# Kernel tuning notes

Measured on AMD Instinct MI355X. Metric: run time of the kernel, lower is better.

The kernel has to match this reference:

```python
import jax, jax.numpy as jnp
import numpy as np

N_NODES = 10000
N_EDGES = 320000


def _graph_conv(x, W, b, src, dst, n):
    # DGL GraphConv, norm='both': D_out^{-1/2} on src side, aggregate, D_in^{-1/2} on dst side,
    # then linear + bias. Degrees clamped at 1 (allow_zero_in_degree=True).
    ones = jnp.ones(src.shape[0], dtype=x.dtype)
    deg_out = jnp.clip(jax.ops.segment_sum(ones, src, num_segments=n), 1.0)
    deg_in = jnp.clip(jax.ops.segment_sum(ones, dst, num_segments=n), 1.0)
    h = x * jax.lax.rsqrt(deg_out)[:, None]          # [n, f] scaled source feats
    agg = jax.ops.segment_sum(h[src], dst, num_segments=n)  # gather + scatter-add
    agg = agg * jax.lax.rsqrt(deg_in)[:, None]
    return agg @ W + b


def setup_inputs() -> dict:
    key = jax.random.key(0)
    ks = jax.random.split(key, 8)
    in_dim, h1, h2 = 512, 256, 128
    features = jax.random.normal(ks[0], (N_NODES, in_dim), dtype=jnp.float32)
    src = jax.random.randint(ks[1], (N_EDGES,), 0, N_NODES)
    dst = jax.random.randint(ks[2], (N_EDGES,), 0, N_NODES)
    noise = jax.random.normal(ks[3], (N_NODES, h2), dtype=jnp.float32)
    W1 = jax.random.normal(ks[4], (in_dim, h1), dtype=jnp.float32) / np.sqrt(in_dim)
    b1 = jnp.zeros((h1,), dtype=jnp.float32)
    W2 = jax.random.normal(ks[5], (h1, h2), dtype=jnp.float32) / np.sqrt(h1)
    b2 = jnp.zeros((h2,), dtype=jnp.float32)
    W3 = jax.random.normal(ks[6], (h1, h2), dtype=jnp.float32) / np.sqrt(h1)
    b3 = jnp.zeros((h2,), dtype=jnp.float32)
    return {"features": features, "src": src, "dst": dst, "noise": noise,
            "W1": W1, "b1": b1, "W2": W2, "b2": b2, "W3": W3, "b3": b3}


def reference(features, src, dst, noise, W1, b1, W2, b2, W3, b3):
    n = features.shape[0]
    h = jax.nn.relu(_graph_conv(features, W1, b1, src, dst, n))
    mean = _graph_conv(h, W2, b2, src, dst, n)
    log_std = _graph_conv(h, W3, b3, src, dst, n)
    z = mean + noise * jnp.exp(log_std)              # reparameterization
    adj_rec = jax.nn.sigmoid(z @ z.T)                # inner-product decoder [N, N]
    return adj_rec
```

## Files before the change

kernel.cpp:

```cpp
#include <hip/hip_runtime.h>
#include <hip/hip_fp16.h>


#define NN 10000
#define NE 320000
#define FD 512
#define H1 256
#define H2 128

typedef _Float16 half8 __attribute__((ext_vector_type(8)));
typedef float f32x4 __attribute__((ext_vector_type(4)));

__device__ __forceinline__ void acc4(float4& a, const float4 v) {
    a.x += v.x; a.y += v.y; a.z += v.z; a.w += v.w;
}

__global__ void k_zero(int* __restrict__ p, int n) {
    int i = blockIdx.x * blockDim.x + threadIdx.x;
    if (i < n) p[i] = 0;
}

__global__ void k_count(const int* __restrict__ src, const int* __restrict__ dst,
                        int* __restrict__ co, int* __restrict__ ci) {
    int e = blockIdx.x * blockDim.x + threadIdx.x;
    if (e < NE) {
        atomicAdd(&co[src[e]], 1);
        atomicAdd(&ci[dst[e]], 1);
    }
}

__global__ __launch_bounds__(1024) void k_scan(const int* __restrict__ ci, const int* __restrict__ co,
                                               int* __restrict__ row_ptr, int* __restrict__ cursor,
                                               float* __restrict__ rs_in, float* __restrict__ rs_out) {
    __shared__ int sm[1024];
    int tid = threadIdx.x;
    const int CH = (NN + 1023) / 1024;
    int base = tid * CH;
    int local[CH];
    int s = 0;
    #pragma unroll
    for (int i = 0; i < CH; ++i) {
        int idx = base + i;
        local[i] = s;
        if (idx < NN) s += ci[idx];
    }
    sm[tid] = s;
    __syncthreads();
    for (int off = 1; off < 1024; off <<= 1) {
        int v = (tid >= off) ? sm[tid - off] : 0;
        __syncthreads();
        sm[tid] += v;
        __syncthreads();
    }
    int excl = sm[tid] - s;
    #pragma unroll
    for (int i = 0; i < CH; ++i) {
        int idx = base + i;
        if (idx < NN) row_ptr[idx] = excl + local[i];
    }
    if (tid == 1023) row_ptr[NN] = sm[1023];
    for (int i = tid; i < NN; i += 1024) {
        int a = ci[i], b = co[i];
        rs_in[i]  = rsqrtf((float)(a > 1 ? a : 1));
        rs_out[i] = rsqrtf((float)(b > 1 ? b : 1));
        cursor[i] = 0;
    }
}

__global__ void k_bucket(const int* __restrict__ src, const int* __restrict__ dst,
                         const int* __restrict__ row_ptr, int* __restrict__ cursor,
                         int* __restrict__ esrc) {
    int e = blockIdx.x * blockDim.x + threadIdx.x;
    if (e < NE) {
        int d = dst[e];
        int p = row_ptr[d] + atomicAdd(&cursor[d], 1);
        esrc[p] = src[e];
    }
}

__global__ __launch_bounds__(256) void k_gemm(
    const float* __restrict__ A, int lda, int M, int K,
    const float* __restrict__ B0, const float* __restrict__ B1, int ldb, int nsplit,
    const float* __restrict__ bias0, const float* __restrict__ bias1,
    const float* __restrict__ ascale, float* __restrict__ C, int ldc) {
    __shared__ __align__(16) float As[16][64];
    __shared__ __align__(16) float Bs[16][64];
    int tid = threadIdx.x;
    int bm = blockIdx.x * 64;
    int bn = blockIdx.y * 64;
    const float* Bp; const float* bp; int bcol;
    if (bn < nsplit) { Bp = B0; bp = bias0; bcol = bn; }
    else             { Bp = B1; bp = bias1; bcol = bn - nsplit; }
    int tm = tid >> 4, tn = tid & 15;
    float acc[4][4] = {};
    int arow = tid >> 2;
    int akq  = tid & 3;
    int brow = tid >> 4;
    int bq   = tid & 15;
    int garow = bm + arow;
    const float* Aptr = (garow < M) ? (A + (size_t)garow * lda) : nullptr;
    float ascl = (ascale && garow < M) ? ascale[garow] : 1.0f;
    for (int k0 = 0; k0 < K; k0 += 16) {
        float4 av = {0.f, 0.f, 0.f, 0.f};
        if (Aptr) av = *(const float4*)(Aptr + k0 + akq * 4);
        av.x *= ascl; av.y *= ascl; av.z *= ascl; av.w *= ascl;
        float4 bv = *(const float4*)(Bp + (size_t)(k0 + brow) * ldb + bcol + bq * 4);
        __syncthreads();
        As[akq * 4 + 0][arow] = av.x;
        As[akq * 4 + 1][arow] = av.y;
        As[akq * 4 + 2][arow] = av.z;
        As[akq * 4 + 3][arow] = av.w;
        *(float4*)&Bs[brow][bq * 4] = bv;
        __syncthreads();
        #pragma unroll
        for (int kk = 0; kk < 16; ++kk) {
            float4 a = *(const float4*)&As[kk][tm * 4];
            float4 b = *(const float4*)&Bs[kk][tn * 4];
            float ar[4] = {a.x, a.y, a.z, a.w};
            float br[4] = {b.x, b.y, b.z, b.w};
            #pragma unroll
            for (int i = 0; i < 4; ++i)
                #pragma unroll
                for (int j = 0; j < 4; ++j)
                    acc[i][j] += ar[i] * br[j];
        }
    }
    float bvv[4];
    #pragma unroll
    for (int j = 0; j < 4; ++j) bvv[j] = bp ? bp[bcol + tn * 4 + j] : 0.0f;
    #pragma unroll
    for (int i = 0; i < 4; ++i) {
        int row = bm + tm * 4 + i;
        if (row < M) {
            float4 v;
            v.x = acc[i][0] + bvv[0];
            v.y = acc[i][1] + bvv[1];
            v.z = acc[i][2] + bvv[2];
            v.w = acc[i][3] + bvv[3];
            *(float4*)(C + (size_t)row * ldc + bn + tn * 4) = v;
        }
    }
}

template <bool FIRST>
__global__ __launch_bounds__(256) void k_agg(const float* __restrict__ in, float* __restrict__ out,
                                             const int* __restrict__ esrc, const int* __restrict__ row_ptr,
                                             const float* __restrict__ rs_in, const float* __restrict__ rs_out,
                                             const float* __restrict__ bias) {
    int node = (blockIdx.x * blockDim.x + threadIdx.x) >> 6;
    int lane = threadIdx.x & 63;
    if (node >= NN) return;
    int beg = row_ptr[node], end = row_ptr[node + 1];
    float4 acc = {0.f, 0.f, 0.f, 0.f};
    int e = beg;
    for (; e + 4 <= end; e += 4) {
        int s0 = esrc[e + 0], s1 = esrc[e + 1], s2 = esrc[e + 2], s3 = esrc[e + 3];
        float4 v0 = ((const float4*)(in + (size_t)s0 * H1))[lane];
        float4 v1 = ((const float4*)(in + (size_t)s1 * H1))[lane];
        float4 v2 = ((const float4*)(in + (size_t)s2 * H1))[lane];
        float4 v3 = ((const float4*)(in + (size_t)s3 * H1))[lane];
        acc4(acc, v0); acc4(acc, v1); acc4(acc, v2); acc4(acc, v3);
    }
    for (; e < end; ++e) {
        float4 v0 = ((const float4*)(in + (size_t)esrc[e] * H1))[lane];
        acc4(acc, v0);
    }
    float si = rs_in[node];
    float4 r;
    r.x = acc.x * si; r.y = acc.y * si; r.z = acc.z * si; r.w = acc.w * si;
    if (FIRST) {
        float4 bb = ((const float4*)bias)[lane];
        float so = rs_out[node];
        r.x = fmaxf(r.x + bb.x, 0.f) * so;
        r.y = fmaxf(r.y + bb.y, 0.f) * so;
        r.z = fmaxf(r.z + bb.z, 0.f) * so;
        r.w = fmaxf(r.w + bb.w, 0.f) * so;
    }
    ((float4*)(out + (size_t)node * H1))[lane] = r;
}

__global__ void k_z(const float* __restrict__ ml, const float* __restrict__ noise,
                    _Float16* __restrict__ z) {
    int i = blockIdx.x * blockDim.x + threadIdx.x;
    if (i < NN * H2) {
        int r = i >> 7, c = i & 127;
        float mean = ml[(size_t)r * 256 + c];
        float ls   = ml[(size_t)r * 256 + 128 + c];
        z[i] = (_Float16)(mean + noise[i] * __expf(ls));
    }
}

__global__ __launch_bounds__(256) void k_decoder(const _Float16* __restrict__ Z, float* __restrict__ out) {
    __shared__ __align__(16) _Float16 As[128][72];
    __shared__ __align__(16) _Float16 Bs[128][72];
    int tid = threadIdx.x;
    int lane = tid & 63;
    int w = tid >> 6;
    int wrow = (w >> 1) * 64;
    int wcol = (w & 1) * 64;
    int rowBase = blockIdx.y * 128;
    int colBase = blockIdx.x * 128;
    f32x4 acc[4][4] = {};
    for (int s = 0; s < 2; ++s) {
        __syncthreads();
        #pragma unroll
        for (int i = 0; i < 4; ++i) {
            int lin = i * 256 + tid;
            int r = lin >> 3, c = lin & 7;
            int4 v = {0, 0, 0, 0};
            int gr = rowBase + r;
            if (gr < NN) v = *(const int4*)(Z + (size_t)gr * H2 + s * 64 + c * 8);
            *(int4*)&As[r][c * 8] = v;
            int4 u = {0, 0, 0, 0};
            int gc = colBase + r;
            if (gc < NN) u = *(const int4*)(Z + (size_t)gc * H2 + s * 64 + c * 8);
            *(int4*)&Bs[r][c * 8] = u;
        }
        __syncthreads();
        #pragma unroll
        for (int kk = 0; kk < 2; ++kk) {
            int kof = kk * 32 + ((lane >> 4) << 3);
            half8 a[4], b[4];
            #pragma unroll
            for (int f = 0; f < 4; ++f) a[f] = *(const half8*)&As[wrow + f * 16 + (lane & 15)][kof];
            #pragma unroll
            for (int f = 0; f < 4; ++f) b[f] = *(const half8*)&Bs[wcol + f * 16 + (lane & 15)][kof];
            #pragma unroll
            for (int i = 0; i < 4; ++i)
                #pragma unroll
                for (int j = 0; j < 4; ++j)
                    acc[i][j] = __builtin_amdgcn_mfma_f32_16x16x32_f16(a[i], b[j], acc[i][j], 0, 0, 0);
        }
    }
    #pragma unroll
    for (int i = 0; i < 4; ++i) {
        int row0 = rowBase + wrow + i * 16 + ((lane >> 4) << 2);
        #pragma unroll
        for (int j = 0; j < 4; ++j) {
            int col = colBase + wcol + j * 16 + (lane & 15);
            if (col < NN) {
                #pragma unroll
                for (int r = 0; r < 4; ++r) {
                    int row = row0 + r;
                    if (row < NN) {
                        float x = acc[i][j][r];
                        float sg = 1.0f / (1.0f + __expf(-x));
                        __builtin_nontemporal_store(sg, out + (size_t)row * NN + col);
                    }
                }
            }
        }
    }
}

extern "C" void kernel_launch(void* const* d_in, const int* in_sizes, int n_in,
                              void* d_out, int out_size, void* d_ws, size_t ws_size,
                              hipStream_t stream) {
    const float* features = (const float*)d_in[0];
    const int*   src      = (const int*)d_in[1];
    const int*   dst      = (const int*)d_in[2];
    const float* noise    = (const float*)d_in[3];
    const float* W1 = (const float*)d_in[4];
    const float* b1 = (const float*)d_in[5];
    const float* W2 = (const float*)d_in[6];
    const float* b2 = (const float*)d_in[7];
    const float* W3 = (const float*)d_in[8];
    const float* b3 = (const float*)d_in[9];
    float* out = (float*)d_out;
    (void)in_sizes; (void)n_in; (void)out_size; (void)ws_size;

    char* ws = (char*)d_ws;
    size_t off = 0;
    auto alloc = [&](size_t bytes) -> void* {
        void* p = ws + off;
        off += (bytes + 255) & ~(size_t)255;
        return p;
    };
    int* degc_out = (int*)alloc(NN * sizeof(int));
    int* degc_in  = (int*)alloc(NN * sizeof(int));
    int* row_ptr  = (int*)alloc((NN + 1) * sizeof(int));
    int* cursor   = (int*)alloc(NN * sizeof(int));
    int* esrc     = (int*)alloc(NE * sizeof(int));
    float* rs_out = (float*)alloc(NN * sizeof(float));
    float* rs_in  = (float*)alloc(NN * sizeof(float));
    float* bufA   = (float*)alloc((size_t)NN * H1 * sizeof(float));
    float* bufB   = (float*)alloc((size_t)NN * H1 * sizeof(float));
    _Float16* Zh  = (_Float16*)alloc((size_t)NN * H2 * sizeof(_Float16));

    k_zero<<<(NN + 255) / 256, 256, 0, stream>>>(degc_out, NN);
    k_zero<<<(NN + 255) / 256, 256, 0, stream>>>(degc_in, NN);
    k_count<<<(NE + 255) / 256, 256, 0, stream>>>(src, dst, degc_out, degc_in);
    k_scan<<<1, 1024, 0, stream>>>(degc_in, degc_out, row_ptr, cursor, rs_in, rs_out);
    k_bucket<<<(NE + 255) / 256, 256, 0, stream>>>(src, dst, row_ptr, cursor, esrc);

    k_gemm<<<dim3((NN + 63) / 64, H1 / 64), 256, 0, stream>>>(
        features, FD, NN, FD, W1, nullptr, H1, H1, nullptr, nullptr, rs_out, bufA, H1);
    k_agg<true><<<NN / 4, 256, 0, stream>>>(bufA, bufB, esrc, row_ptr, rs_in, rs_out, b1);
    k_agg<false><<<NN / 4, 256, 0, stream>>>(bufB, bufA, esrc, row_ptr, rs_in, nullptr, nullptr);
    k_gemm<<<dim3((NN + 63) / 64, 4), 256, 0, stream>>>(
        bufA, H1, NN, H1, W2, W3, H2, H2, b2, b3, nullptr, bufB, 256);
    k_z<<<(NN * H2 + 255) / 256, 256, 0, stream>>>(bufB, noise, Zh);
    k_decoder<<<dim3((NN + 127) / 128, (NN + 127) / 128), 256, 0, stream>>>(Zh, out);
}
```

Baseline: 686.0 us.

## Replace FP32 SIMT GEMMs with split-FP16 MFMA GEMMs using pre-transposed weights

Replaces the scalar FP32 tiled GEMM with an MFMA-based kernel. Each FP32 operand is split into high and low FP16 halves and three 16x16x32 f16 MFMAs per tile pair recover near-FP32 accuracy. A new kernel pre-transposes and splits W1 and the concatenated W2/W3 into FP16 hi/lo arrays and merges the biases. The two degree-zeroing launches are also fused into one. This trades triple MFMA work and an extra cast launch for much higher matrix throughput than FP32 FMA loops.

New measurement: 660.7 us. -3.7%, faster.

```diff
diff --git a/kernel.cpp b/kernel.cpp
--- a/kernel.cpp
+++ b/kernel.cpp
@@ -9,15 +9,16 @@
 #define H2 128
 
 typedef _Float16 half8 __attribute__((ext_vector_type(8)));
+typedef _Float16 half4 __attribute__((ext_vector_type(4)));
 typedef float f32x4 __attribute__((ext_vector_type(4)));
 
 __device__ __forceinline__ void acc4(float4& a, const float4 v) {
     a.x += v.x; a.y += v.y; a.z += v.z; a.w += v.w;
 }
 
-__global__ void k_zero(int* __restrict__ p, int n) {
+__global__ void k_zero2(int* __restrict__ a, int* __restrict__ b, int n) {
     int i = blockIdx.x * blockDim.x + threadIdx.x;
-    if (i < n) p[i] = 0;
+    if (i < n) { a[i] = 0; b[i] = 0; }
 }
 
 __global__ void k_count(const int* __restrict__ src, const int* __restrict__ dst,
@@ -78,66 +79,107 @@
     }
 }
 
-__global__ __launch_bounds__(256) void k_gemm(
-    const float* __restrict__ A, int lda, int M, int K,
-    const float* __restrict__ B0, const float* __restrict__ B1, int ldb, int nsplit,
-    const float* __restrict__ bias0, const float* __restrict__ bias1,
-    const float* __restrict__ ascale, float* __restrict__ C, int ldc) {
-    __shared__ __align__(16) float As[16][64];
-    __shared__ __align__(16) float Bs[16][64];
+__global__ void k_castW(const float* __restrict__ W1, const float* __restrict__ W2,
+                        const float* __restrict__ W3, const float* __restrict__ b2,
+                        const float* __restrict__ b3,
+                        _Float16* __restrict__ W1Th, _Float16* __restrict__ W1Tl,
+                        _Float16* __restrict__ WcTh, _Float16* __restrict__ WcTl,
+                        float* __restrict__ biasC) {
+    int idx = blockIdx.x * blockDim.x + threadIdx.x;
+    if (idx < FD * H1) {
+        int k = idx >> 8, n = idx & 255;
+        float v = W1[idx];
+        _Float16 h = (_Float16)v;
+        W1Th[n * FD + k] = h;
+        W1Tl[n * FD + k] = (_Float16)(v - (float)h);
+    } else if (idx < FD * H1 + H1 * H1) {
+        int j = idx - FD * H1;
+        int k = j >> 8, n = j & 255;
+        float v = (n < H2) ? W2[k * H2 + n] : W3[k * H2 + (n - H2)];
+        _Float16 h = (_Float16)v;
+        WcTh[n * H1 + k] = h;
+        WcTl[n * H1 + k] = (_Float16)(v - (float)h);
+        if (k == 0) biasC[n] = (n < H2) ? b2[n] : b3[n - H2];
+    }
+}
+
+template <int K>
+__global__ __launch_bounds__(256) void k_gemm16(
+    const float* __restrict__ A, const float* __restrict__ ascale,
+    const _Float16* __restrict__ BTh, const _Float16* __restrict__ BTl,
+    const float* __restrict__ bias, float* __restrict__ C, int M) {
+    __shared__ __align__(16) _Float16 Ahs[64][72];
+    __shared__ __align__(16) _Float16 Als[64][72];
+    __shared__ __align__(16) _Float16 Bhs[64][72];
+    __shared__ __align__(16) _Float16 Bls[64][72];
     int tid = threadIdx.x;
-    int bm = blockIdx.x * 64;
-    int bn = blockIdx.y * 64;
-    const float* Bp; const float* bp; int bcol;
-    if (bn < nsplit) { Bp = B0; bp = bias0; bcol = bn; }
-    else             { Bp = B1; bp = bias1; bcol = bn - nsplit; }
-    int tm = tid >> 4, tn = tid & 15;
-    float acc[4][4] = {};
-    int arow = tid >> 2;
-    int akq  = tid & 3;
-    int brow = tid >> 4;
-    int bq   = tid & 15;
-    int garow = bm + arow;
-    const float* Aptr = (garow < M) ? (A + (size_t)garow * lda) : nullptr;
-    float ascl = (ascale && garow < M) ? ascale[garow] : 1.0f;
-    for (int k0 = 0; k0 < K; k0 += 16) {
-        float4 av = {0.f, 0.f, 0.f, 0.f};
-        if (Aptr) av = *(const float4*)(Aptr + k0 + akq * 4);
-        av.x *= ascl; av.y *= ascl; av.z *= ascl; av.w *= ascl;
-        float4 bv = *(const float4*)(Bp + (size_t)(k0 + brow) * ldb + bcol + bq * 4);
-        __syncthreads();
-        As[akq * 4 + 0][arow] = av.x;
-        As[akq * 4 + 1][arow] = av.y;
-        As[akq * 4 + 2][arow] = av.z;
-        As[akq * 4 + 3][arow] = av.w;
-        *(float4*)&Bs[brow][bq * 4] = bv;
-        __syncthreads();
-        #pragma unroll
-        for (int kk = 0; kk < 16; ++kk) {
-            float4 a = *(const float4*)&As[kk][tm * 4];
-            float4 b = *(const float4*)&Bs[kk][tn * 4];
-            float ar[4] = {a.x, a.y, a.z, a.w};
-            float br[4] = {b.x, b.y, b.z, b.w};
-            #pragma unroll
-            for (int i = 0; i < 4; ++i)
+    int lane = tid & 63;
+    int w = tid >> 6;
+    int wr = (w >> 1) * 32, wc = (w & 1) * 32;
+    int bm = blockIdx.x * 64, bn = blockIdx.y * 64;
+    f32x4 acc[2][2] = {};
+    for (int k0 = 0; k0 < K; k0 += 64) {
+        __syncthreads();
+        #pragma unroll
+        for (int i = 0; i < 4; ++i) {
+            int lin = i * 256 + tid;
+            int r = lin >> 4, c = lin & 15;
+            int gr = bm + r;
+            float4 v = {0.f, 0.f, 0.f, 0.f};
+            float s = 1.0f;
+            if (gr < M) {
+                v = *(const float4*)(A + (size_t)gr * K + k0 + c * 4);
+                if (ascale) s = ascale[gr];
+            }
+            v.x *= s; v.y *= s; v.z *= s; v.w *= s;
+            half4 hh = { (_Float16)v.x, (_Float16)v.y, (_Float16)v.z, (_Float16)v.w };
+            half4 ll = { (_Float16)(v.x - (float)hh.x), (_Float16)(v.y - (float)hh.y),
+                         (_Float16)(v.z - (float)hh.z), (_Float16)(v.w - (float)hh.w) };
+            *(half4*)&Ahs[r][c * 4] = hh;
+            *(half4*)&Als[r][c * 4] = ll;
+        }
+        #pragma unroll
+        for (int i = 0; i < 2; ++i) {
+            int lin = i * 256 + tid;
+            int r = lin >> 3, c = lin & 7;
+            *(int4*)&Bhs[r][c * 8] = *(const int4*)(BTh + (size_t)(bn + r) * K + k0 + c * 8);
+            *(int4*)&Bls[r][c * 8] = *(const int4*)(BTl + (size_t)(bn + r) * K + k0 + c * 8);
+        }
+        __syncthreads();
+        #pragma unroll
+        for (int ks = 0; ks < 2; ++ks) {
+            int kof = ks * 32 + ((lane >> 4) << 3);
+            half8 ah[2], al[2], bh[2], bl[2];
+            #pragma unroll
+            for (int f = 0; f < 2; ++f) {
+                ah[f] = *(const half8*)&Ahs[wr + f * 16 + (lane & 15)][kof];
+                al[f] = *(const half8*)&Als[wr + f * 16 + (lane & 15)][kof];
+                bh[f] = *(const half8*)&Bhs[wc + f * 16 + (lane & 15)][kof];
+                bl[f] = *(const half8*)&Bls[wc + f * 16 + (lane & 15)][kof];
+            }
+            #pragma unroll
+            for (int i = 0; i < 2; ++i)
                 #pragma unroll
-                for (int j = 0; j < 4; ++j)
-                    acc[i][j] += ar[i] * br[j];
-        }
-    }
-    float bvv[4];
+                for (int j = 0; j < 2; ++j) {
+                    acc[i][j] = __builtin_amdgcn_mfma_f32_16x16x32_f16(ah[i], bh[j], acc[i][j], 0, 0, 0);
+                    acc[i][j] = __builtin_amdgcn_mfma_f32_16x16x32_f16(ah[i], bl[j], acc[i][j], 0, 0, 0);
+                    acc[i][j] = __builtin_amdgcn_mfma_f32_16x16x32_f16(al[i], bh[j], acc[i][j], 0, 0, 0);
+                }
+        }
+    }
+    int quad = lane >> 4, c16 = lane & 15;
     #pragma unroll
-    for (int j = 0; j < 4; ++j) bvv[j] = bp ? bp[bcol + tn * 4 + j] : 0.0f;
-    #pragma unroll
-    for (int i = 0; i < 4; ++i) {
-        int row = bm + tm * 4 + i;
-        if (row < M) {
-            float4 v;
-            v.x = acc[i][0] + bvv[0];
-            v.y = acc[i][1] + bvv[1];
-            v.z = acc[i][2] + bvv[2];
-            v.w = acc[i][3] + bvv[3];
-            *(float4*)(C + (size_t)row * ldc + bn + tn * 4) = v;
+    for (int i = 0; i < 2; ++i) {
+        int row0 = bm + wr + i * 16 + quad * 4;
+        #pragma unroll
+        for (int j = 0; j < 2; ++j) {
+            int col = bn + wc + j * 16 + c16;
+            float bb = bias ? bias[col] : 0.0f;
+            #pragma unroll
+            for (int r = 0; r < 4; ++r) {
+                int row = row0 + r;
+                if (row < M) C[(size_t)row * H1 + col] = acc[i][j][r] + bb;
+            }
         }
     }
 }
@@ -283,22 +325,28 @@
     int* esrc     = (int*)alloc(NE * sizeof(int));
     float* rs_out = (float*)alloc(NN * sizeof(float));
     float* rs_in  = (float*)alloc(NN * sizeof(float));
+    _Float16* W1Th = (_Float16*)alloc((size_t)H1 * FD * sizeof(_Float16));
+    _Float16* W1Tl = (_Float16*)alloc((size_t)H1 * FD * sizeof(_Float16));
+    _Float16* WcTh = (_Float16*)alloc((size_t)H1 * H1 * sizeof(_Float16));
+    _Float16* WcTl = (_Float16*)alloc((size_t)H1 * H1 * sizeof(_Float16));
+    float* biasC  = (float*)alloc(H1 * sizeof(float));
     float* bufA   = (float*)alloc((size_t)NN * H1 * sizeof(float));
     float* bufB   = (float*)alloc((size_t)NN * H1 * sizeof(float));
     _Float16* Zh  = (_Float16*)alloc((size_t)NN * H2 * sizeof(_Float16));
 
-    k_zero<<<(NN + 255) / 256, 256, 0, stream>>>(degc_out, NN);
-    k_zero<<<(NN + 255) / 256, 256, 0, stream>>>(degc_in, NN);
+    k_zero2<<<(NN + 255) / 256, 256, 0, stream>>>(degc_out, degc_in, NN);
     k_count<<<(NE + 255) / 256, 256, 0, stream>>>(src, dst, degc_out, degc_in);
     k_scan<<<1, 1024, 0, stream>>>(degc_in, degc_out, row_ptr, cursor, rs_in, rs_out);
     k_bucket<<<(NE + 255) / 256, 256, 0, stream>>>(src, dst, row_ptr, cursor, esrc);
-
-    k_gemm<<<dim3((NN + 63) / 64, H1 / 64), 256, 0, stream>>>(
-        features, FD, NN, FD, W1, nullptr, H1, H1, nullptr, nullptr, rs_out, bufA, H1);
+    k_castW<<<(FD * H1 + H1 * H1 + 255) / 256, 256, 0, stream>>>(
+        W1, W2, W3, b2, b3, W1Th, W1Tl, WcTh, WcTl, biasC);
+
+    k_gemm16<FD><<<dim3((NN + 63) / 64, H1 / 64), 256, 0, stream>>>(
+        features, rs_out, W1Th, W1Tl, nullptr, bufA, NN);
     k_agg<true><<<NN / 4, 256, 0, stream>>>(bufA, bufB, esrc, row_ptr, rs_in, rs_out, b1);
     k_agg<false><<<NN / 4, 256, 0, stream>>>(bufB, bufA, esrc, row_ptr, rs_in, nullptr, nullptr);
-    k_gemm<<<dim3((NN + 63) / 64, 4), 256, 0, stream>>>(
-        bufA, H1, NN, H1, W2, W3, H2, H2, b2, b3, nullptr, bufB, 256);
+    k_gemm16<H1><<<dim3((NN + 63) / 64, H1 / 64), 256, 0, stream>>>(
+        bufA, nullptr, WcTh, WcTl, biasC, bufB, NN);
     k_z<<<(NN * H2 + 255) / 256, 256, 0, stream>>>(bufB, noise, Zh);
     k_decoder<<<dim3((NN + 127) / 128, (NN + 127) / 128), 256, 0, stream>>>(Zh, out);
 }
```
